# Optimization experiments

Measured on AMD Instinct MI355X. Metric: run time of the kernel, lower is better.

Reference implementation:

```python
import jax, jax.numpy as jnp
import numpy as np

D_MODEL = 1024
NUM_HEADS = 16
DEPTH = D_MODEL // NUM_HEADS


def setup_inputs() -> dict:
    key = jax.random.key(0)
    ks = jax.random.split(key, 11)
    B, S = 4, 2048
    scale = 1.0 / np.sqrt(D_MODEL)
    inp = {
        "q": jax.random.normal(ks[0], (B, S, D_MODEL), jnp.float32),
        "k": jax.random.normal(ks[1], (B, S, D_MODEL), jnp.float32),
        "v": jax.random.normal(ks[2], (B, S, D_MODEL), jnp.float32),
        # Linear params (weight stored [out, in] like torch; applied as x @ W.T + b)
        "wq_w": jax.random.normal(ks[3], (D_MODEL, D_MODEL), jnp.float32) * scale,
        "wq_b": jnp.zeros((D_MODEL,), jnp.float32),
        "wk_w": jax.random.normal(ks[4], (D_MODEL, D_MODEL), jnp.float32) * scale,
        "wk_b": jnp.zeros((D_MODEL,), jnp.float32),
        "wv_w": jax.random.normal(ks[5], (D_MODEL, D_MODEL), jnp.float32) * scale,
        "wv_b": jnp.zeros((D_MODEL,), jnp.float32),
        "wo_w": jax.random.normal(ks[6], (D_MODEL, D_MODEL), jnp.float32) * scale,
        "wo_b": jnp.zeros((D_MODEL,), jnp.float32),
    }
    return inp


def _split_heads(x, B, S):
    # [B, S, D] -> [B, H, S, depth]
    return x.reshape(B, S, NUM_HEADS, DEPTH).transpose(0, 2, 1, 3)


def reference(q, k, v, wq_w, wq_b, wk_w, wk_b, wv_w, wv_b, wo_w, wo_b):
    B, S, _ = q.shape
    qh = _split_heads(q @ wq_w.T + wq_b, B, S)
    kh = _split_heads(k @ wk_w.T + wk_b, B, S)
    vh = _split_heads(v @ wv_w.T + wv_b, B, S)
    # scaled dot-product attention: [B, H, Sq, Sk]
    scores = jnp.einsum("bhqd,bhkd->bhqk", qh, kh) / jnp.sqrt(
        jnp.asarray(DEPTH, qh.dtype))
    attn = jax.nn.softmax(scores, axis=-1)
    ctx = jnp.einsum("bhqk,bhkd->bhqd", attn, vh)
    # [B, H, S, depth] -> [B, S, D]
    ctx = ctx.transpose(0, 2, 1, 3).reshape(B, S, D_MODEL)
    return ctx @ wo_w.T + wo_b
```

## Files before the change

kernel.cpp:

```cpp
#include <hip/hip_runtime.h>
#include <hip/hip_bf16.h>

typedef __attribute__((ext_vector_type(8))) short bf16x8;
typedef __attribute__((ext_vector_type(4))) short bf16x4;
typedef __attribute__((ext_vector_type(4))) float f32x4;
typedef __attribute__((address_space(3))) ushort lds_ushort;

#define MFMA32(a, b, c) __builtin_amdgcn_mfma_f32_16x16x32_bf16(a, b, c, 0, 0, 0)
#if __has_builtin(__builtin_amdgcn_mfma_f32_16x16x16bf16_1k)
#define HAVE_MFMA16K 1
#define MFMA16K(a, b, c) __builtin_amdgcn_mfma_f32_16x16x16bf16_1k(a, b, c, 0, 0, 0)
#else
#define HAVE_MFMA16K 0
#endif

#define ASYNC16(g, l)                                                          \
    __builtin_amdgcn_global_load_lds(                                          \
        (const __attribute__((address_space(1))) unsigned int*)(g),            \
        (__attribute__((address_space(3))) unsigned int*)(l), 16, 0, 0)

#define TR16(dst, addr, OFF)                                                   \
    asm volatile("ds_read_b64_tr_b16 %0, %1 offset:%2"                         \
                 : "=v"(dst) : "v"(addr), "i"(OFF))

__device__ __forceinline__ ushort f2bf(float f) {
    __hip_bfloat16 h = __float2bfloat16(f);
    return *reinterpret_cast<ushort*>(&h);
}
__device__ __forceinline__ uint cvtpk(float a, float b) {
    uint r;
    asm("v_cvt_pk_bf16_f32 %0, %1, %2" : "=v"(r) : "v"(a), "v"(b));
    return r;
}

#define QSCALE 0.18033688011112042f

struct CvtArgs { const float* s[4]; ushort* d[4]; int nb[4]; };

__global__ __launch_bounds__(256) void cvtk(CvtArgs a) {
    const int z = blockIdx.y;
    if ((int)blockIdx.x >= a.nb[z]) return;
    const float* s = a.s[z];
    ushort* d = a.d[z];
    const size_t i = (size_t)blockIdx.x * 2048 + threadIdx.x * 8;
    float4 f0 = *(const float4*)&s[i];
    float4 f1 = *(const float4*)&s[i + 4];
    *(ushort4*)&d[i]     = make_ushort4(f2bf(f0.x), f2bf(f0.y), f2bf(f0.z), f2bf(f0.w));
    *(ushort4*)&d[i + 4] = make_ushort4(f2bf(f1.x), f2bf(f1.y), f2bf(f1.z), f2bf(f1.w));
}

struct GemmArgs {
    const ushort* X[3]; const float* Xf[3]; const ushort* W[3];
    const float* B[3]; void* O[3]; int mode[3]; int xf32[3]; float scale[3];
};

__global__ __launch_bounds__(256) void gemm3(GemmArgs g) {
    __shared__ __attribute__((aligned(16))) ushort As[2][128][32];
    __shared__ __attribute__((aligned(16))) ushort Bs[2][128][32];

    const int z = blockIdx.z;
    const ushort* __restrict__ W = g.W[z];
    const float*  __restrict__ bias = g.B[z];
    const int mode = g.mode[z];
    const float scale = g.scale[z];

    const int tid  = threadIdx.x;
    const int lane = tid & 63;
    const int wave = tid >> 6;
    const int quad = lane >> 4;
    const int l16  = lane & 15;
    const int wm   = (wave >> 1) * 64;
    const int wn   = (wave & 1) * 64;

    const int flat = blockIdx.x + 8 * blockIdx.y;
    const int t    = (flat & 7) * 64 + (flat >> 3);
    const int m0   = (t >> 3) * 128;
    const int n0   = (t & 7) * 128;

    f32x4 acc[4][4];
#pragma unroll
    for (int i = 0; i < 4; i++)
#pragma unroll
        for (int j = 0; j < 4; j++) acc[i][j] = (f32x4)0.0f;

    auto stageB = [&](int buf, int k0) {
#pragma unroll
        for (int j = 0; j < 2; j++) {
            const int c   = j * 256 + tid;
            const int r   = c >> 2;
            const int col = (c & 3) * 8;
            ASYNC16(&W[(size_t)(n0 + r) * 1024 + k0 + col],
                    &Bs[buf][0][0] + (size_t)(j * 256 + wave * 64) * 8);
        }
    };

    if (g.xf32[z]) {
        const float* __restrict__ Xf = g.Xf[z];
        const int r0 = tid >> 2, cq = (tid & 3) * 8;
        float4 a0, a1, b0, b1;
        auto loadA = [&](int k0) {
            a0 = *(const float4*)&Xf[(size_t)(m0 + r0) * 1024 + k0 + cq];
            a1 = *(const float4*)&Xf[(size_t)(m0 + r0) * 1024 + k0 + cq + 4];
            b0 = *(const float4*)&Xf[(size_t)(m0 + 64 + r0) * 1024 + k0 + cq];
            b1 = *(const float4*)&Xf[(size_t)(m0 + 64 + r0) * 1024 + k0 + cq + 4];
        };
        auto writeA = [&](int buf) {
            uint4 w;
            w.x = cvtpk(a0.x, a0.y); w.y = cvtpk(a0.z, a0.w);
            w.z = cvtpk(a1.x, a1.y); w.w = cvtpk(a1.z, a1.w);
            *(uint4*)&As[buf][r0][cq] = w;
            w.x = cvtpk(b0.x, b0.y); w.y = cvtpk(b0.z, b0.w);
            w.z = cvtpk(b1.x, b1.y); w.w = cvtpk(b1.z, b1.w);
            *(uint4*)&As[buf][64 + r0][cq] = w;
        };

        loadA(0);
        writeA(0);
        stageB(0, 0);
        loadA(32);

        int cur = 0;
        for (int k0 = 0; k0 < 1024; k0 += 32) {
            __syncthreads();
            if (k0 + 32 < 1024) {
                writeA(cur ^ 1);
                stageB(cur ^ 1, k0 + 32);
            }
            if (k0 + 64 < 1024) loadA(k0 + 64);

            bf16x8 af[4], bfr[4];
#pragma unroll
            for (int i = 0; i < 4; i++)
                af[i] = *(const bf16x8*)&As[cur][wm + i * 16 + l16][quad * 8];
#pragma unroll
            for (int j = 0; j < 4; j++)
                bfr[j] = *(const bf16x8*)&Bs[cur][wn + j * 16 + l16][quad * 8];
#pragma unroll
            for (int i = 0; i < 4; i++)
#pragma unroll
                for (int j = 0; j < 4; j++)
                    acc[i][j] = MFMA32(af[i], bfr[j], acc[i][j]);
            cur ^= 1;
        }
    } else {
        const ushort* __restrict__ X = g.X[z];
        auto stageA = [&](int buf, int k0) {
#pragma unroll
            for (int j = 0; j < 2; j++) {
                const int c   = j * 256 + tid;
                const int r   = c >> 2;
                const int col = (c & 3) * 8;
                ASYNC16(&X[(size_t)(m0 + r) * 1024 + k0 + col],
                        &As[buf][0][0] + (size_t)(j * 256 + wave * 64) * 8);
            }
        };
        stageA(0, 0);
        stageB(0, 0);
        int cur = 0;
        for (int k0 = 0; k0 < 1024; k0 += 32) {
            __syncthreads();
            if (k0 + 32 < 1024) {
                stageA(cur ^ 1, k0 + 32);
                stageB(cur ^ 1, k0 + 32);
            }
            bf16x8 af[4], bfr[4];
#pragma unroll
            for (int i = 0; i < 4; i++)
                af[i] = *(const bf16x8*)&As[cur][wm + i * 16 + l16][quad * 8];
#pragma unroll
            for (int j = 0; j < 4; j++)
                bfr[j] = *(const bf16x8*)&Bs[cur][wn + j * 16 + l16][quad * 8];
#pragma unroll
            for (int i = 0; i < 4; i++)
#pragma unroll
                for (int j = 0; j < 4; j++)
                    acc[i][j] = MFMA32(af[i], bfr[j], acc[i][j]);
            cur ^= 1;
        }
    }

#pragma unroll
    for (int i = 0; i < 4; i++) {
#pragma unroll
        for (int j = 0; j < 4; j++) {
            const int n  = n0 + wn + j * 16 + l16;
            const float bb = bias[n];
#pragma unroll
            for (int r = 0; r < 4; r++) {
                const int m = m0 + wm + i * 16 + quad * 4 + r;
                const float val = (acc[i][j][r] + bb) * scale;
                if (mode == 2) {
                    ((float*)g.O[z])[(size_t)m * 1024 + n] = val;
                } else {
                    const int bat = m >> 11, s = m & 2047, h = n >> 6, d = n & 63;
                    ((ushort*)g.O[z])[((size_t)((bat * 16 + h) * 2048 + s)) * 64 + d]
                        = f2bf(val);
                }
            }
        }
    }
}

__global__ __launch_bounds__(256, 4) void attn(
    const ushort* __restrict__ Qp, const ushort* __restrict__ Kp,
    const ushort* __restrict__ Vp, ushort* __restrict__ ctx)
{
    __shared__ __attribute__((aligned(16))) ushort Ks[2][2 * 64 * 32];
    __shared__ __attribute__((aligned(16))) ushort Vs[2][64 * 64];

    const int tid  = threadIdx.x;
    const int lane = tid & 63;
    const int wave = tid >> 6;
    const int quad = lane >> 4;
    const int l16  = lane & 15;

    const int id = blockIdx.x;
    const int bh = (id & 7) * 8 + ((id >> 3) & 7);
    const int q0 = (id >> 6) * 128;
    const int b  = bh >> 4, h = bh & 15;

    const ushort* Qg = Qp + ((size_t)bh * 2048 + q0) * 64;
    const ushort* Kg = Kp + (size_t)bh * 2048 * 64;
    const ushort* Vg = Vp + (size_t)bh * 2048 * 64;

    bf16x8 aq[2][2];
#pragma unroll
    for (int st = 0; st < 2; st++)
#pragma unroll
        for (int kk = 0; kk < 2; kk++)
            aq[st][kk] = *(const bf16x8*)&Qg[(size_t)(wave * 32 + st * 16 + l16) * 64
                                            + kk * 32 + quad * 8];

    f32x4 o[2][4];
#pragma unroll
    for (int st = 0; st < 2; st++)
#pragma unroll
        for (int jd = 0; jd < 4; jd++) o[st][jd] = (f32x4)0.0f;
#if HAVE_MFMA16K
    f32x4 ls[2] = {(f32x4)0.0f, (f32x4)0.0f};
    union { uint u[2]; bf16x4 v; } ones;
    ones.u[0] = 0x3F803F80u; ones.u[1] = 0x3F803F80u;
#else
    float lsum[2] = {0.f, 0.f};
#endif

    auto stage = [&](int buf, int n0) {
#pragma unroll
        for (int j = 0; j < 2; j++) {
            const int c    = j * 256 + tid;
            const int colq = c & 3;
            const int row  = (c >> 2) & 63;
            const int half = c >> 8;
            ASYNC16(&Kg[(size_t)(n0 + row) * 64 + half * 32 + colq * 8],
                    &Ks[buf][0] + (size_t)(j * 256 + wave * 64) * 8);
        }
#pragma unroll
        for (int j = 0; j < 2; j++) {
            const int c   = j * 256 + tid;
            const int key = ((c >> 5) << 2) | ((c >> 1) & 3);
            const int d   = (((c >> 3) & 3) << 4) | ((c & 1) << 3);
            ASYNC16(&Vg[(size_t)(n0 + key) * 64 + d],
                    &Vs[buf][0] + (size_t)(j * 256 + wave * 64) * 8);
        }
    };

    stage(0, 0);
    int cur = 0;

    for (int n0 = 0; n0 < 2048; n0 += 64) {
        __syncthreads();
        if (n0 + 64 < 2048) stage(cur ^ 1, n0 + 64);

        uint pk[4][2][2];
#pragma unroll
        for (int kb = 0; kb < 4; kb++) {
            bf16x8 kf0 = *(const bf16x8*)&Ks[cur][(size_t)(kb * 16 + l16) * 32 + quad * 8];
            bf16x8 kf1 = *(const bf16x8*)&Ks[cur][(size_t)(64 + kb * 16 + l16) * 32 + quad * 8];
#pragma unroll
            for (int st = 0; st < 2; st++) {
                f32x4 s = (f32x4)0.0f;
                s = MFMA32(kf0, aq[st][0], s);
                s = MFMA32(kf1, aq[st][1], s);
                float e0 = __builtin_amdgcn_exp2f(s[0]);
                float e1 = __builtin_amdgcn_exp2f(s[1]);
                float e2 = __builtin_amdgcn_exp2f(s[2]);
                float e3 = __builtin_amdgcn_exp2f(s[3]);
                pk[kb][st][0] = cvtpk(e0, e1);
                pk[kb][st][1] = cvtpk(e2, e3);
#if !HAVE_MFMA16K
                lsum[st] += (e0 + e1) + (e2 + e3);
#endif
            }
        }

#if HAVE_MFMA16K
        const lds_ushort* vp = (const lds_ushort*)&Vs[cur][0] + quad * 256 + l16 * 4;
        bf16x4 vf[4][4];
#define TRISSUE(JD)                                                            \
        TR16(vf[JD][0], vp, (JD) * 128 + 0);                                   \
        TR16(vf[JD][1], vp, (JD) * 128 + 2048);                                \
        TR16(vf[JD][2], vp, (JD) * 128 + 4096);                                \
        TR16(vf[JD][3], vp, (JD) * 128 + 6144);
        TRISSUE(0) TRISSUE(1) TRISSUE(2) TRISSUE(3)

#pragma unroll
        for (int kb = 0; kb < 4; kb++) {
#pragma unroll
            for (int st = 0; st < 2; st++) {
                union { uint u[2]; bf16x4 v; } pf;
                pf.u[0] = pk[kb][st][0];
                pf.u[1] = pk[kb][st][1];
                ls[st] = MFMA16K(pf.v, ones.v, ls[st]);
            }
        }

#define PVWAIT(N)                                                              \
        asm volatile("s_waitcnt lgkmcnt(" #N ")" ::: "memory");                \
        __builtin_amdgcn_sched_barrier(0);
#define PVJD(JD)                                                               \
        _Pragma("unroll")                                                      \
        for (int kb = 0; kb < 4; kb++) {                                       \
            _Pragma("unroll")                                                  \
            for (int st = 0; st < 2; st++) {                                   \
                union { uint u[2]; bf16x4 v; } pf;                             \
                pf.u[0] = pk[kb][st][0];                                       \
                pf.u[1] = pk[kb][st][1];                                       \
                o[st][JD] = MFMA16K(pf.v, vf[JD][kb], o[st][JD]);              \
            }                                                                  \
        }
        __builtin_amdgcn_s_setprio(1);
        PVWAIT(12) PVJD(0)
        PVWAIT(8)  PVJD(1)
        PVWAIT(4)  PVJD(2)
        PVWAIT(0)  PVJD(3)
        __builtin_amdgcn_s_setprio(0);
#else
        const int addr0 = 4 * ((2 * (quad & 1)) * 16 + l16);
        const int addr1 = addr0 + 64;
#pragma unroll
        for (int kt = 0; kt < 2; kt++) {
            bf16x8 apf[2];
#pragma unroll
            for (int st = 0; st < 2; st++) {
                union { uint u[4]; bf16x8 v; } t;
#pragma unroll
                for (int j = 0; j < 4; j++) {
                    uint src = (quad & 2) ? pk[kt * 2 + 1][st][j & 1]
                                          : pk[kt * 2][st][j & 1];
                    t.u[j] = (uint)__builtin_amdgcn_ds_bpermute(
                        (j >> 1) ? addr1 : addr0, (int)src);
                }
                apf[st] = t.v;
            }
#pragma unroll
            for (int jd = 0; jd < 4; jd++) {
                union { ushort s[8]; bf16x8 v; } vv;
#pragma unroll
                for (int e = 0; e < 8; e++) {
                    const int key = kt * 32 + quad * 8 + e;
                    const int d   = jd * 16 + l16;
                    vv.s[e] = Vs[cur][(key >> 2) * 256 + (d >> 4) * 64
                                      + (key & 3) * 16 + (d & 15)];
                }
#pragma unroll
                for (int st = 0; st < 2; st++)
                    o[st][jd] = MFMA32(apf[st], vv.v, o[st][jd]);
            }
        }
#endif
        cur ^= 1;
    }

#if HAVE_MFMA16K
#pragma unroll
    for (int st = 0; st < 2; st++) {
        float inv[4];
#pragma unroll
        for (int r = 0; r < 4; r++) inv[r] = 1.0f / ls[st][r];
#pragma unroll
        for (int jd = 0; jd < 4; jd++) {
#pragma unroll
            for (int r = 0; r < 4; r++) {
                const int s = q0 + wave * 32 + st * 16 + quad * 4 + r;
                ctx[((size_t)(b * 2048 + s)) * 1024 + h * 64 + jd * 16 + l16] =
                    f2bf(o[st][jd][r] * inv[r]);
            }
        }
    }
#else
#pragma unroll
    for (int st = 0; st < 2; st++) {
        float lsv = lsum[st];
        lsv += __shfl_xor(lsv, 16, 64);
        lsv += __shfl_xor(lsv, 32, 64);
        float inv[4];
#pragma unroll
        for (int r = 0; r < 4; r++)
            inv[r] = 1.0f / __shfl(lsv, quad * 4 + r, 64);
#pragma unroll
        for (int jd = 0; jd < 4; jd++) {
#pragma unroll
            for (int r = 0; r < 4; r++) {
                const int s = q0 + wave * 32 + st * 16 + quad * 4 + r;
                ctx[((size_t)(b * 2048 + s)) * 1024 + h * 64 + jd * 16 + l16] =
                    f2bf(o[st][jd][r] * inv[r]);
            }
        }
    }
#endif
}

extern "C" void kernel_launch(void* const* d_in, const int* in_sizes, int n_in,
                              void* d_out, int out_size, void* d_ws, size_t ws_size,
                              hipStream_t stream) {
    const float* q    = (const float*)d_in[0];
    const float* k    = (const float*)d_in[1];
    const float* v    = (const float*)d_in[2];
    const float* wq_w = (const float*)d_in[3];
    const float* wq_b = (const float*)d_in[4];
    const float* wk_w = (const float*)d_in[5];
    const float* wk_b = (const float*)d_in[6];
    const float* wv_w = (const float*)d_in[7];
    const float* wv_b = (const float*)d_in[8];
    const float* wo_w = (const float*)d_in[9];
    const float* wo_b = (const float*)d_in[10];
    float* out = (float*)d_out;

    const size_t NE = (size_t)4 * 2048 * 1024;
    const size_t NW = (size_t)1024 * 1024;
    const size_t need_fused = (4 * NE + 4 * NW) * 2;

    dim3 blk(256);

    if (ws_size >= need_fused) {
        ushort* Wq = (ushort*)d_ws;
        ushort* Wk = Wq + NW;
        ushort* Wv = Wk + NW;
        ushort* Wo = Wv + NW;
        ushort* Qp = Wo + NW;
        ushort* Kp = Qp + NE;
        ushort* Vp = Kp + NE;
        ushort* ctx = Vp + NE;

        CvtArgs ca;
        ca.s[0]=wq_w; ca.d[0]=Wq; ca.nb[0]=512;
        ca.s[1]=wk_w; ca.d[1]=Wk; ca.nb[1]=512;
        ca.s[2]=wv_w; ca.d[2]=Wv; ca.nb[2]=512;
        ca.s[3]=wo_w; ca.d[3]=Wo; ca.nb[3]=512;
        cvtk<<<dim3(512, 4), blk, 0, stream>>>(ca);

        GemmArgs ga;
        ga.Xf[0]=q; ga.Xf[1]=k; ga.Xf[2]=v;
        ga.X[0]=ga.X[1]=ga.X[2]=nullptr;
        ga.W[0]=Wq; ga.W[1]=Wk; ga.W[2]=Wv;
        ga.B[0]=wq_b; ga.B[1]=wk_b; ga.B[2]=wv_b;
        ga.O[0]=Qp; ga.O[1]=Kp; ga.O[2]=Vp;
        ga.mode[0]=ga.mode[1]=ga.mode[2]=0;
        ga.xf32[0]=ga.xf32[1]=ga.xf32[2]=1;
        ga.scale[0]=QSCALE; ga.scale[1]=1.0f; ga.scale[2]=1.0f;
        gemm3<<<dim3(8, 64, 3), blk, 0, stream>>>(ga);

        attn<<<dim3(1024), blk, 0, stream>>>(Qp, Kp, Vp, ctx);

        GemmArgs go;
        for (int i = 0; i < 3; i++) {
            go.X[i]=ctx; go.Xf[i]=nullptr; go.W[i]=Wo; go.B[i]=wo_b;
            go.O[i]=out; go.mode[i]=2; go.xf32[i]=0; go.scale[i]=1.0f;
        }
        gemm3<<<dim3(8, 64, 1), blk, 0, stream>>>(go);
    } else {
        ushort* Qp  = (ushort*)d_ws;
        ushort* Kp  = Qp + NE;
        ushort* Vp  = Kp + NE;
        ushort* ctx = Vp + NE;
        ushort* Wb  = ctx + NE;

        const float* xs[3] = {q, k, v};
        const float* ws[3] = {wq_w, wk_w, wv_w};
        const float* bs[3] = {wq_b, wk_b, wv_b};
        ushort* os[3] = {Qp, Kp, Vp};
        for (int p = 0; p < 3; p++) {
            CvtArgs c;
            c.s[0]=ws[p]; c.d[0]=Wb; c.nb[0]=512;
            for (int i = 1; i < 4; i++) { c.s[i]=ws[p]; c.d[i]=Wb; c.nb[i]=0; }
            cvtk<<<dim3(512, 1), blk, 0, stream>>>(c);
            GemmArgs gg;
            for (int i = 0; i < 3; i++) {
                gg.Xf[i]=xs[p]; gg.X[i]=nullptr; gg.W[i]=Wb; gg.B[i]=bs[p];
                gg.O[i]=os[p]; gg.mode[i]=0; gg.xf32[i]=1;
                gg.scale[i]=(p == 0) ? QSCALE : 1.0f;
            }
            gemm3<<<dim3(8, 64, 1), blk, 0, stream>>>(gg);
        }

        attn<<<dim3(1024), blk, 0, stream>>>(Qp, Kp, Vp, ctx);

        CvtArgs c;
        c.s[0]=wo_w; c.d[0]=Wb; c.nb[0]=512;
        for (int i = 1; i < 4; i++) { c.s[i]=wo_w; c.d[i]=Wb; c.nb[i]=0; }
        cvtk<<<dim3(512, 1), blk, 0, stream>>>(c);
        GemmArgs go;
        for (int i = 0; i < 3; i++) {
            go.X[i]=ctx; go.Xf[i]=nullptr; go.W[i]=Wb; go.B[i]=wo_b;
            go.O[i]=out; go.mode[i]=2; go.xf32[i]=0; go.scale[i]=1.0f;
        }
        gemm3<<<dim3(8, 64, 1), blk, 0, stream>>>(go);
    }
}
```

Measured before the change: 366.6 us.

## Stage fp32 activations via async LDS loads and narrow GEMM N-tile to 64

The projection GEMM now copies fp32 activation tiles straight into LDS with async global-to-LDS loads, using an XOR-swizzled layout, and converts them to bf16 when reading fragments, instead of loading into registers and converting before the LDS write. The block tile shrinks from 128x128 to 128x64, so the grid has twice as many blocks and each wave accumulates half as many tiles. The aim is to overlap the activation fetch asynchronously and raise occupancy or block count. The trade-off is more LDS for the fp32 A tile, conversion work repeated by both N-waves, and A data read again across more N-tiles.

```diff
diff --git a/kernel.cpp b/kernel.cpp
--- a/kernel.cpp
+++ b/kernel.cpp
@@ -55,8 +55,8 @@
 };
 
 __global__ __launch_bounds__(256) void gemm3(GemmArgs g) {
-    __shared__ __attribute__((aligned(16))) ushort As[2][128][32];
-    __shared__ __attribute__((aligned(16))) ushort Bs[2][128][32];
+    __shared__ __attribute__((aligned(16))) float  Asf[2][128][32];
+    __shared__ __attribute__((aligned(16))) ushort Bs[2][64][32];
 
     const int z = blockIdx.z;
     const ushort* __restrict__ W = g.W[z];
@@ -70,88 +70,84 @@
     const int quad = lane >> 4;
     const int l16  = lane & 15;
     const int wm   = (wave >> 1) * 64;
-    const int wn   = (wave & 1) * 64;
-
-    const int flat = blockIdx.x + 8 * blockIdx.y;
-    const int t    = (flat & 7) * 64 + (flat >> 3);
-    const int m0   = (t >> 3) * 128;
-    const int n0   = (t & 7) * 128;
-
-    f32x4 acc[4][4];
+    const int wn   = (wave & 1) * 32;
+
+    const int flat = blockIdx.x + 16 * blockIdx.y;
+    const int t    = (flat & 7) * 128 + (flat >> 3);
+    const int m0   = (t >> 4) * 128;
+    const int n0   = (t & 15) * 64;
+
+    f32x4 acc[4][2];
 #pragma unroll
     for (int i = 0; i < 4; i++)
 #pragma unroll
-        for (int j = 0; j < 4; j++) acc[i][j] = (f32x4)0.0f;
+        for (int j = 0; j < 2; j++) acc[i][j] = (f32x4)0.0f;
 
     auto stageB = [&](int buf, int k0) {
-#pragma unroll
-        for (int j = 0; j < 2; j++) {
-            const int c   = j * 256 + tid;
-            const int r   = c >> 2;
-            const int col = (c & 3) * 8;
-            ASYNC16(&W[(size_t)(n0 + r) * 1024 + k0 + col],
-                    &Bs[buf][0][0] + (size_t)(j * 256 + wave * 64) * 8);
-        }
+        const int row = tid >> 2, colq = tid & 3;
+        ASYNC16(&W[(size_t)(n0 + row) * 1024 + k0 + colq * 8],
+                &Bs[buf][0][0] + (size_t)(wave * 64) * 8);
     };
 
     if (g.xf32[z]) {
         const float* __restrict__ Xf = g.Xf[z];
-        const int r0 = tid >> 2, cq = (tid & 3) * 8;
-        float4 a0, a1, b0, b1;
-        auto loadA = [&](int k0) {
-            a0 = *(const float4*)&Xf[(size_t)(m0 + r0) * 1024 + k0 + cq];
-            a1 = *(const float4*)&Xf[(size_t)(m0 + r0) * 1024 + k0 + cq + 4];
-            b0 = *(const float4*)&Xf[(size_t)(m0 + 64 + r0) * 1024 + k0 + cq];
-            b1 = *(const float4*)&Xf[(size_t)(m0 + 64 + r0) * 1024 + k0 + cq + 4];
+        auto stageA = [&](int buf, int k0) {
+#pragma unroll
+            for (int j = 0; j < 4; j++) {
+                const int c    = j * 256 + tid;
+                const int row  = c >> 3;
+                const int srcg = (c & 7) ^ (row & 7);
+                ASYNC16(&Xf[(size_t)(m0 + row) * 1024 + k0 + srcg * 4],
+                        &Asf[buf][0][0] + (size_t)(j * 256 + wave * 64) * 4);
+            }
         };
-        auto writeA = [&](int buf) {
-            uint4 w;
-            w.x = cvtpk(a0.x, a0.y); w.y = cvtpk(a0.z, a0.w);
-            w.z = cvtpk(a1.x, a1.y); w.w = cvtpk(a1.z, a1.w);
-            *(uint4*)&As[buf][r0][cq] = w;
-            w.x = cvtpk(b0.x, b0.y); w.y = cvtpk(b0.z, b0.w);
-            w.z = cvtpk(b1.x, b1.y); w.w = cvtpk(b1.z, b1.w);
-            *(uint4*)&As[buf][64 + r0][cq] = w;
-        };
-
-        loadA(0);
-        writeA(0);
+
+        stageA(0, 0);
         stageB(0, 0);
-        loadA(32);
-
         int cur = 0;
         for (int k0 = 0; k0 < 1024; k0 += 32) {
             __syncthreads();
             if (k0 + 32 < 1024) {
-                writeA(cur ^ 1);
+                stageA(cur ^ 1, k0 + 32);
                 stageB(cur ^ 1, k0 + 32);
             }
-            if (k0 + 64 < 1024) loadA(k0 + 64);
-
-            bf16x8 af[4], bfr[4];
+            const int sw = l16 & 7;
+            bf16x8 af[4], bfr[2];
+#pragma unroll
+            for (int i = 0; i < 4; i++) {
+                const int row = wm + i * 16 + l16;
+                f32x4 f0 = *(const f32x4*)&Asf[cur][row][((quad * 2) ^ sw) * 4];
+                f32x4 f1 = *(const f32x4*)&Asf[cur][row][((quad * 2 + 1) ^ sw) * 4];
+                union { uint u[4]; bf16x8 v; } p;
+                p.u[0] = cvtpk(f0[0], f0[1]);
+                p.u[1] = cvtpk(f0[2], f0[3]);
+                p.u[2] = cvtpk(f1[0], f1[1]);
+                p.u[3] = cvtpk(f1[2], f1[3]);
+                af[i] = p.v;
+            }
+#pragma unroll
+            for (int j = 0; j < 2; j++)
+                bfr[j] = *(const bf16x8*)&Bs[cur][wn + j * 16 + l16][quad * 8];
 #pragma unroll
             for (int i = 0; i < 4; i++)
-                af[i] = *(const bf16x8*)&As[cur][wm + i * 16 + l16][quad * 8];
-#pragma unroll
-            for (int j = 0; j < 4; j++)
-                bfr[j] = *(const bf16x8*)&Bs[cur][wn + j * 16 + l16][quad * 8];
-#pragma unroll
-            for (int i = 0; i < 4; i++)
-#pragma unroll
-                for (int j = 0; j < 4; j++)
+#pragma unroll
+                for (int j = 0; j < 2; j++)
                     acc[i][j] = MFMA32(af[i], bfr[j], acc[i][j]);
             cur ^= 1;
         }
     } else {
         const ushort* __restrict__ X = g.X[z];
+        ushort* As0 = (ushort*)&Asf[0][0][0];
+        ushort* As1 = (ushort*)&Asf[1][0][0];
         auto stageA = [&](int buf, int k0) {
+            ushort* dst = buf ? As1 : As0;
 #pragma unroll
             for (int j = 0; j < 2; j++) {
                 const int c   = j * 256 + tid;
-                const int r   = c >> 2;
+                const int row = c >> 2;
                 const int col = (c & 3) * 8;
-                ASYNC16(&X[(size_t)(m0 + r) * 1024 + k0 + col],
-                        &As[buf][0][0] + (size_t)(j * 256 + wave * 64) * 8);
+                ASYNC16(&X[(size_t)(m0 + row) * 1024 + k0 + col],
+                        dst + (size_t)(j * 256 + wave * 64) * 8);
             }
         };
         stageA(0, 0);
@@ -163,17 +159,18 @@
                 stageA(cur ^ 1, k0 + 32);
                 stageB(cur ^ 1, k0 + 32);
             }
-            bf16x8 af[4], bfr[4];
+            const ushort* As = cur ? As1 : As0;
+            bf16x8 af[4], bfr[2];
 #pragma unroll
             for (int i = 0; i < 4; i++)
-                af[i] = *(const bf16x8*)&As[cur][wm + i * 16 + l16][quad * 8];
-#pragma unroll
-            for (int j = 0; j < 4; j++)
+                af[i] = *(const bf16x8*)&As[(size_t)(wm + i * 16 + l16) * 32 + quad * 8];
+#pragma unroll
+            for (int j = 0; j < 2; j++)
                 bfr[j] = *(const bf16x8*)&Bs[cur][wn + j * 16 + l16][quad * 8];
 #pragma unroll
             for (int i = 0; i < 4; i++)
 #pragma unroll
-                for (int j = 0; j < 4; j++)
+                for (int j = 0; j < 2; j++)
                     acc[i][j] = MFMA32(af[i], bfr[j], acc[i][j]);
             cur ^= 1;
         }
@@ -182,7 +179,7 @@
 #pragma unroll
     for (int i = 0; i < 4; i++) {
 #pragma unroll
-        for (int j = 0; j < 4; j++) {
+        for (int j = 0; j < 2; j++) {
             const int n  = n0 + wn + j * 16 + l16;
             const float bb = bias[n];
 #pragma unroll
@@ -458,7 +455,7 @@
         ga.mode[0]=ga.mode[1]=ga.mode[2]=0;
         ga.xf32[0]=ga.xf32[1]=ga.xf32[2]=1;
         ga.scale[0]=QSCALE; ga.scale[1]=1.0f; ga.scale[2]=1.0f;
-        gemm3<<<dim3(8, 64, 3), blk, 0, stream>>>(ga);
+        gemm3<<<dim3(16, 64, 3), blk, 0, stream>>>(ga);
 
         attn<<<dim3(1024), blk, 0, stream>>>(Qp, Kp, Vp, ctx);
 
@@ -467,7 +464,7 @@
             go.X[i]=ctx; go.Xf[i]=nullptr; go.W[i]=Wo; go.B[i]=wo_b;
             go.O[i]=out; go.mode[i]=2; go.xf32[i]=0; go.scale[i]=1.0f;
         }
-        gemm3<<<dim3(8, 64, 1), blk, 0, stream>>>(go);
+        gemm3<<<dim3(16, 64, 1), blk, 0, stream>>>(go);
     } else {
         ushort* Qp  = (ushort*)d_ws;
         ushort* Kp  = Qp + NE;
@@ -490,7 +487,7 @@
                 gg.O[i]=os[p]; gg.mode[i]=0; gg.xf32[i]=1;
                 gg.scale[i]=(p == 0) ? QSCALE : 1.0f;
             }
-            gemm3<<<dim3(8, 64, 1), blk, 0, stream>>>(gg);
+            gemm3<<<dim3(16, 64, 1), blk, 0, stream>>>(gg);
         }
 
         attn<<<dim3(1024), blk, 0, stream>>>(Qp, Kp, Vp, ctx);
@@ -504,6 +501,6 @@
             go.X[i]=ctx; go.Xf[i]=nullptr; go.W[i]=Wb; go.B[i]=wo_b;
             go.O[i]=out; go.mode[i]=2; go.xf32[i]=0; go.scale[i]=1.0f;
         }
-        gemm3<<<dim3(8, 64, 1), blk, 0, stream>>>(go);
+        gemm3<<<dim3(16, 64, 1), blk, 0, stream>>>(go);
     }
 }
```

Result: slower. 392.3 us (+7.0%).
